# Optimization experiments

Measured on AMD Instinct MI355X. Metric: run time of the kernel, lower is better.

The kernel has to match this reference:

```python
import jax, jax.numpy as jnp
import numpy as np

NUM_HEADS = 12
DIM_HEAD = 64
SCALE = DIM_HEAD ** -0.5
LOG2PI = float(np.log(2.0 * np.pi))


def setup_inputs() -> dict:
    key = jax.random.key(0)
    k1, k2, k3, k4 = jax.random.split(key, 4)
    b, n, e = 2, 2048, 768
    inner = NUM_HEADS * DIM_HEAD
    return {
        "x": jax.random.normal(k1, (b, n, e), dtype=jnp.float32),
        "w_qkv": jax.random.normal(k2, (e, 3 * inner), dtype=jnp.float32) * (e ** -0.5),
        "w_out": jax.random.normal(k3, (inner, e), dtype=jnp.float32) * (inner ** -0.5),
        "b_out": jax.random.normal(k4, (e,), dtype=jnp.float32) * 0.02,
    }


def reference(x, w_qkv, w_out, b_out):
    b, n, _ = x.shape
    h, d = NUM_HEADS, DIM_HEAD
    qkv = x @ w_qkv  # (b, n, 3*h*d)
    q, k, v = jnp.split(qkv, 3, axis=-1)
    # (b, n, h*d) -> (b, h, n, d)
    to_heads = lambda t: t.reshape(b, n, h, d).transpose(0, 2, 1, 3)
    q, k, v = to_heads(q), to_heads(k), to_heads(v)

    dots = jnp.einsum("bhid,bhjd->bhij", q, k) * SCALE  # (b, h, n, n)
    attn = jax.nn.softmax(dots, axis=-1)
    product = jnp.einsum("bhij,bhjd->bhid", attn, v)  # (b, h, n, d)

    # cross-head statistics (torch.var is unbiased -> ddof=1)
    mean = jnp.mean(product, axis=1, keepdims=True)           # (b, 1, n, d)
    variance = jnp.var(product, axis=1, ddof=1, keepdims=True)  # (b, 1, n, d)

    log_probs = -0.5 * (LOG2PI + jnp.log(variance)
                        - 0.5 * (product - mean) ** 2 / variance)
    log_probs = jnp.sum(log_probs, axis=-1) \
        - jnp.sum(jnp.log(jnp.sqrt(variance)), axis=-1)  # (b, h, n)

    # second attn-weighted matmul, weighted by per-(b,h,n) log-likelihood
    out = jnp.einsum("bhij,bhjd->bhid", log_probs[..., None] * attn, v)
    out = out.transpose(0, 2, 1, 3).reshape(b, n, h * d)  # (b, n, h*d)
    return out @ w_out + b_out
```

## Files before the change

kernel.cpp:

```cpp
#include <hip/hip_runtime.h>

#define BB    2
#define NCTX  2048
#define EDIM  768
#define HH    12
#define DH    64
#define NQKV  2304
#define QSZ   (BB*HH*NCTX*DH)
#define GK    768
#define SCALE 0.125f
#define LOG2PI 1.8378770664093453f

typedef __bf16 bf16x8 __attribute__((ext_vector_type(8)));
typedef float  f32x4  __attribute__((ext_vector_type(4)));
typedef float  f32x16 __attribute__((ext_vector_type(16)));

#define GLOAD_LDS16(g, l)                                      \
  __builtin_amdgcn_global_load_lds(                            \
      (const __attribute__((address_space(1))) void*)(g),      \
      (__attribute__((address_space(3))) void*)(l), 16, 0, 0)

__global__ __launch_bounds__(256)
void cvt_x(const float* __restrict__ x, __bf16* __restrict__ xbf, int n8) {
  int i = blockIdx.x*256 + threadIdx.x;
  if (i < n8) {
    float4 a = *(const float4*)(x + (size_t)i*8);
    float4 b = *(const float4*)(x + (size_t)i*8 + 4);
    bf16x8 o;
    o[0]=(__bf16)a.x; o[1]=(__bf16)a.y; o[2]=(__bf16)a.z; o[3]=(__bf16)a.w;
    o[4]=(__bf16)b.x; o[5]=(__bf16)b.y; o[6]=(__bf16)b.z; o[7]=(__bf16)b.w;
    *(bf16x8*)(xbf + (size_t)i*8) = o;
  }
}

__device__ __forceinline__
void cvt_T_tile(const float* __restrict__ W, __bf16* __restrict__ WT,
                int R, int C, int c0, int r0, int t) {
  __shared__ float ts[32][33];
  const int rr = t >> 5, cc = t & 31;
  #pragma unroll
  for (int i = 0; i < 4; ++i)
    ts[rr + i*8][cc] = W[(size_t)(r0 + rr + i*8)*C + c0 + cc];
  __syncthreads();
  #pragma unroll
  for (int i = 0; i < 4; ++i)
    WT[(size_t)(c0 + rr + i*8)*R + r0 + cc] = (__bf16)ts[cc][rr + i*8];
}

__global__ __launch_bounds__(256)
void cvt_T_both(const float* __restrict__ wqkv, const float* __restrict__ wout,
                __bf16* __restrict__ wqkvT, __bf16* __restrict__ woutT) {
  int b = blockIdx.x;
  if (b < 1728) {
    cvt_T_tile(wqkv, wqkvT, GK, NQKV, (b % 72)*32, (b / 72)*32, threadIdx.x);
  } else {
    b -= 1728;
    cvt_T_tile(wout, woutT, GK, EDIM, (b % 24)*32, (b / 24)*32, threadIdx.x);
  }
}

#define GEMM_CORE(Aa, Bb, acc)                                               \
  const int lane = tid & 63, w = tid >> 6;                                   \
  const int l15 = lane & 15, g = lane >> 4;                                  \
  const int wr = w >> 1, wc = w & 1;                                         \
  const int lrow16 = lane >> 2;                                              \
  const int lsl = (lane & 3) ^ ((lane >> 3) & 3);                            \
  f32x4 acc[4][4];                                                           \
  _Pragma("unroll")                                                          \
  for (int i = 0; i < 4; ++i)                                                \
    _Pragma("unroll")                                                        \
    for (int j = 0; j < 4; ++j) acc[i][j] = (f32x4){0.f,0.f,0.f,0.f};        \
  const __bf16* Asrc = (Aa) + (size_t)(w*32 + lrow16)*GK + lsl*8;            \
  const __bf16* Bsrc = (Bb) + (size_t)(w*32 + lrow16)*GK + lsl*8;            \
  char* dstA = smem + w*2048;                                                \
  char* dstB = smem + 8192 + w*2048;                                         \
  _Pragma("unroll")                                                          \
  for (int i = 0; i < 2; ++i) {                                              \
    GLOAD_LDS16(Asrc + (size_t)i*16*GK, dstA + i*1024);                      \
    GLOAD_LDS16(Bsrc + (size_t)i*16*GK, dstB + i*1024);                      \
  }                                                                          \
  for (int ki = 0; ki < GK/32; ++ki) {                                       \
    const int c = ki & 1;                                                    \
    __syncthreads();                        \
    if (ki + 1 < GK/32) {                                                    \
      _Pragma("unroll")                                                      \
      for (int i = 0; i < 2; ++i) {                                          \
        GLOAD_LDS16(Asrc + (size_t)i*16*GK + (ki+1)*32,                      \
                    dstA + (1-c)*16384 + i*1024);                            \
        GLOAD_LDS16(Bsrc + (size_t)i*16*GK + (ki+1)*32,                      \
                    dstB + (1-c)*16384 + i*1024);                            \
      }                                                                      \
    }                                                                        \
    const char* Asc = smem + c*16384;                                        \
    const char* Bsc = Asc + 8192;                                            \
    bf16x8 af[4], bf[4];                                                     \
    _Pragma("unroll")                                                        \
    for (int mf = 0; mf < 4; ++mf) {                                         \
      int m = wr*64 + mf*16 + l15;                                           \
      af[mf] = *(const bf16x8*)(Asc + m*64 + ((g*16) ^ (((m>>1)&3)<<4)));    \
    }                                                                        \
    _Pragma("unroll")                                                        \
    for (int nf = 0; nf < 4; ++nf) {                                         \
      int n = wc*64 + nf*16 + l15;                                           \
      bf[nf] = *(const bf16x8*)(Bsc + n*64 + ((g*16) ^ (((n>>1)&3)<<4)));    \
    }                                                                        \
    __builtin_amdgcn_s_setprio(1);                                           \
    _Pragma("unroll")                                                        \
    for (int mf = 0; mf < 4; ++mf)                                           \
      _Pragma("unroll")                                                      \
      for (int nf = 0; nf < 4; ++nf)                                         \
        acc[mf][nf] = __builtin_amdgcn_mfma_f32_16x16x32_bf16(               \
            af[mf], bf[nf], acc[mf][nf], 0, 0, 0);                           \
    __builtin_amdgcn_s_setprio(0);                                           \
  }

__global__ __launch_bounds__(256)
void gemm_qkv_mfma(const __bf16* __restrict__ A, const __bf16* __restrict__ BT,
                   __bf16* __restrict__ qb, __bf16* __restrict__ kb,
                   __bf16* __restrict__ vtb) {
  __shared__ __align__(16) char smem[2*16384];
  const int tid = threadIdx.x;
  const int xcd = blockIdx.x & 7, local = blockIdx.x >> 3;
  const int mb = (xcd & 3)*8 + local/9;
  const int nb = (xcd >> 2)*9 + local%9;
  const int m0 = mb*128, n0 = nb*128;
  GEMM_CORE(A + (size_t)m0*GK, BT + (size_t)n0*GK, acc)
  #pragma unroll
  for (int mf = 0; mf < 4; ++mf)
    #pragma unroll
    for (int nf = 0; nf < 4; ++nf)
      #pragma unroll
      for (int r = 0; r < 4; ++r) {
        int m = m0 + wr*64 + mf*16 + g*4 + r;
        int c = n0 + wc*64 + nf*16 + l15;
        int b_ = m >> 11, ii = m & 2047;
        int t = c / 768;
        int rem = c - t*768;
        int head = rem >> 6, dd = rem & 63;
        float val = acc[mf][nf][r];
        if (t == 0)
          qb[((size_t)(b_*HH + head)*NCTX + ii)*DH + dd] = (__bf16)(val * SCALE);
        else if (t == 1)
          kb[((size_t)(b_*HH + head)*NCTX + ii)*DH + dd] = (__bf16)val;
        else
          vtb[((size_t)(b_*HH + head)*DH + dd)*NCTX + ii] = (__bf16)val;
      }
}

__global__ __launch_bounds__(512)
void attn_mfma(const __bf16* __restrict__ Q, const __bf16* __restrict__ K,
               const __bf16* __restrict__ Vg, float* __restrict__ P) {
  __shared__ __align__(16) char smem[2*32768];
  const int bh  = blockIdx.x;
  const int q0  = blockIdx.y * 128;
  const int tid = threadIdx.x;
  const int w = tid >> 6, lane = tid & 63;
  const int wq = w & 3, wk = w >> 2;
  const int l31 = lane & 31, hi = lane >> 5;
  const __bf16* Qb = Q  + (size_t)bh * NCTX * DH;
  const __bf16* Kb = K  + (size_t)bh * NCTX * DH;
  const __bf16* Vb = Vg + (size_t)bh * DH * NCTX;

  bf16x8 qa[4];
  {
    const __bf16* qr = Qb + (size_t)(q0 + wq*32 + l31)*DH + hi*8;
    #pragma unroll
    for (int s = 0; s < 4; ++s) qa[s] = *(const bf16x8*)(qr + s*16);
  }
  bf16x8 ones;
  #pragma unroll
  for (int j = 0; j < 8; ++j) ones[j] = (__bf16)1.0f;

  f32x16 oacc[2], lacc, zero16;
  #pragma unroll
  for (int i = 0; i < 16; ++i)
    { oacc[0][i] = 0.f; oacc[1][i] = 0.f; lacc[i] = 0.f; zero16[i] = 0.f; }

  const int lrow  = lane >> 3;
  const int lslot = (lane & 7) ^ lrow;
  const bool isK = (w < 4);
  const int wg = isK ? w : (w - 4);
  const __bf16* src0 = isK ? (Kb + (size_t)(wg*16 + lrow)*DH   + lslot*8)
                           : (Vb + (size_t)(wg*16 + lrow)*NCTX + lslot*8);
  const int dstoff = (isK ? 0 : 8192) + wg*2048;

  #define STAGE(kk_, s_) do {                                                 \
    char* sb = smem + (s_)*32768 + dstoff;                                    \
    if (isK) {                                                                \
      GLOAD_LDS16(src0 + (size_t)(kk_)*DH,          sb);                      \
      GLOAD_LDS16(src0 + (size_t)(kk_)*DH + 512,    sb + 1024);               \
      GLOAD_LDS16(src0 + (size_t)(kk_)*DH + 4096,   sb + 16384);              \
      GLOAD_LDS16(src0 + (size_t)(kk_)*DH + 4608,   sb + 16384 + 1024);       \
    } else {                                                                  \
      GLOAD_LDS16(src0 + (kk_),                     sb);                      \
      GLOAD_LDS16(src0 + (kk_) + 8*NCTX,            sb + 1024);               \
      GLOAD_LDS16(src0 + (kk_) + 64,                sb + 16384);              \
      GLOAD_LDS16(src0 + (kk_) + 64 + 8*NCTX,       sb + 16384 + 1024);       \
    }                                                                         \
  } while (0)

  #define ATTN_TILE(TB) do {                                                  \
    const char* Kl = (TB);                                                    \
    const char* Vt = (TB) + 8192;                                             \
    f32x16 sacc;                                                              \
    __builtin_amdgcn_s_setprio(1);                                            \
    {                                                                         \
      const int key = wk*32 + l31;                                            \
      const char* kbase = Kl + key*128;                                       \
      const int swz = (key&7) << 4;                                           \
      bf16x8 kf = *(const bf16x8*)(kbase + ((hi*16) ^ swz));                  \
      sacc = __builtin_amdgcn_mfma_f32_32x32x16_bf16(kf, qa[0], zero16, 0, 0, 0); \
      _Pragma("unroll")                                                       \
      for (int s = 1; s < 4; ++s) {                                           \
        kf = *(const bf16x8*)(kbase + ((s*32 + hi*16) ^ swz));                \
        sacc = __builtin_amdgcn_mfma_f32_32x32x16_bf16(kf, qa[s], sacc, 0, 0, 0); \
      }                                                                       \
    }                                                                         \
    __builtin_amdgcn_s_setprio(0);                                            \
    unsigned px0, px1, px2, px3, px4, px5, px6, px7;                          \
    {                                                                         \
      float e[16];                                                            \
      _Pragma("unroll")                                                       \
      for (int r = 0; r < 16; ++r) e[r] = __expf(sacc[r]);                    \
      CVTPK(px0, e[0],  e[1]);  CVTPK(px1, e[2],  e[3]);                      \
      CVTPK(px2, e[4],  e[5]);  CVTPK(px3, e[6],  e[7]);                      \
      CVTPK(px4, e[8],  e[9]);  CVTPK(px5, e[10], e[11]);                     \
      CVTPK(px6, e[12], e[13]); CVTPK(px7, e[14], e[15]);                     \
      asm("v_permlane32_swap_b32 %0, %1" : "+v"(px0), "+v"(px2));             \
      asm("v_permlane32_swap_b32 %0, %1" : "+v"(px1), "+v"(px3));             \
      asm("v_permlane32_swap_b32 %0, %1" : "+v"(px4), "+v"(px6));             \
      asm("v_permlane32_swap_b32 %0, %1" : "+v"(px5), "+v"(px7));             \
    }                                                                         \
    union PF { unsigned u[4]; bf16x8 v; };                                    \
    PF pf0, pf1;                                                              \
    pf0.u[0]=px0; pf0.u[1]=px1; pf0.u[2]=px2; pf0.u[3]=px3;                   \
    pf1.u[0]=px4; pf1.u[1]=px5; pf1.u[2]=px6; pf1.u[3]=px7;                   \
    __builtin_amdgcn_s_setprio(1);                                            \
    _Pragma("unroll")                                                         \
    for (int s = 0; s < 2; ++s) {                                             \
      bf16x8 pf = s ? pf1.v : pf0.v;                                          \
      lacc = __builtin_amdgcn_mfma_f32_32x32x16_bf16(pf, ones, lacc, 0, 0, 0);\
      _Pragma("unroll")                                                       \
      for (int nf = 0; nf < 2; ++nf) {                                        \
        int d = nf*32 + l31;                                                  \
        bf16x8 vf = *(const bf16x8*)(Vt + d*128 +                             \
            (((wk*32 + s*16 + hi*8)*2) ^ ((d&7)<<4)));                        \
        oacc[nf] = __builtin_amdgcn_mfma_f32_32x32x16_bf16(pf, vf, oacc[nf], 0, 0, 0); \
      }                                                                       \
    }                                                                         \
    __builtin_amdgcn_s_setprio(0);                                            \
  } while (0)

  #define CVTPK(dst, a, b) \
    asm("v_cvt_pk_bf16_f32 %0, %1, %2" : "=v"(dst) : "v"(a), "v"(b))

  STAGE(0, 0);

  for (int ts = 0; ts < NCTX/128; ++ts) {
    const int s = ts & 1;
    __syncthreads();
    if (ts + 1 < NCTX/128) STAGE((ts+1)*128, 1-s);
    const char* sb = smem + s*32768;
    ATTN_TILE(sb);
    ATTN_TILE(sb + 16384);
  }
  #undef STAGE
  #undef ATTN_TILE
  #undef CVTPK

  __syncthreads();
  float* scrO = (float*)smem;
  float* scrL = (float*)(smem + 32768);
  if (wk == 1) {
    #pragma unroll
    for (int nf = 0; nf < 2; ++nf)
      #pragma unroll
      for (int r = 0; r < 16; ++r)
        scrO[((wq*2 + nf)*16 + r)*64 + lane] = oacc[nf][r];
    #pragma unroll
    for (int r = 0; r < 16; ++r)
      scrL[(wq*16 + r)*64 + lane] = lacc[r];
  }
  __syncthreads();
  if (wk == 0) {
    #pragma unroll
    for (int r = 0; r < 16; ++r) {
      float linv = 1.0f / (lacc[r] + scrL[(wq*16 + r)*64 + lane]);
      int q = q0 + wq*32 + (r&3) + 8*(r>>2) + 4*hi;
      #pragma unroll
      for (int nf = 0; nf < 2; ++nf) {
        float o = oacc[nf][r] + scrO[((wq*2 + nf)*16 + r)*64 + lane];
        P[((size_t)bh*NCTX + q)*DH + nf*32 + l31] = o * linv;
      }
    }
  }
}

__global__ __launch_bounds__(256)
void stats_scale(const float* __restrict__ P, __bf16* __restrict__ Pbf) {
  const int bi = blockIdx.x*4 + (threadIdx.x >> 6);
  const int b_ = bi >> 11, i = bi & 2047;
  const int d = threadIdx.x & 63;
  const size_t hstride = (size_t)NCTX * DH;
  const size_t base = ((size_t)(b_*HH) * NCTX + i) * DH + d;
  float x[HH];
  #pragma unroll
  for (int h = 0; h < HH; ++h) x[h] = P[base + h*hstride];
  float sum = 0.f;
  #pragma unroll
  for (int h = 0; h < HH; ++h) sum += x[h];
  float mean = sum * (1.0f/12.0f);
  float ss = 0.f;
  #pragma unroll
  for (int h = 0; h < HH; ++h) { float t = x[h]-mean; ss += t*t; }
  float var = ss * (1.0f/11.0f);
  float lv = logf(var);
  float inv = 0.25f / var;
  __bf16* orow = Pbf + (size_t)bi * GK + d;
  #pragma unroll
  for (int h = 0; h < HH; ++h) {
    float t = x[h] - mean;
    float part = -0.5f*LOG2PI - lv + t*t*inv;
    #pragma unroll
    for (int off = 32; off; off >>= 1) part += __shfl_xor(part, off);
    orow[h*DH] = (__bf16)(part * x[h]);
  }
}

__global__ __launch_bounds__(256)
void gemm_out_mfma(const __bf16* __restrict__ A, const __bf16* __restrict__ BT,
                   const float* __restrict__ bias, float* __restrict__ out) {
  __shared__ __align__(16) char smem[2*16384];
  const int tid = threadIdx.x;
  const int xcd = blockIdx.x & 7, local = blockIdx.x >> 3;
  const int mb = (xcd & 3)*8 + local/3;
  const int nb = (xcd >> 2)*3 + local%3;
  const int m0 = mb*128, n0 = nb*128;
  GEMM_CORE(A + (size_t)m0*GK, BT + (size_t)n0*GK, acc)
  #pragma unroll
  for (int mf = 0; mf < 4; ++mf)
    #pragma unroll
    for (int nf = 0; nf < 4; ++nf)
      #pragma unroll
      for (int r = 0; r < 4; ++r) {
        int m = m0 + wr*64 + mf*16 + g*4 + r;
        int c = n0 + wc*64 + nf*16 + l15;
        out[(size_t)m*EDIM + c] = acc[mf][nf][r] + bias[c];
      }
}

extern "C" void kernel_launch(void* const* d_in, const int* in_sizes, int n_in,
                              void* d_out, int out_size, void* d_ws, size_t ws_size,
                              hipStream_t stream) {
  const float* x     = (const float*)d_in[0];
  const float* w_qkv = (const float*)d_in[1];
  const float* w_out = (const float*)d_in[2];
  const float* b_out = (const float*)d_in[3];
  float* out = (float*)d_out;

  __bf16* xbf   = (__bf16*)d_ws;
  __bf16* wqkvT = xbf   + (size_t)BB*NCTX*GK;
  __bf16* woutT = wqkvT + (size_t)NQKV*GK;
  __bf16* qb    = woutT + (size_t)EDIM*GK;
  __bf16* kb    = qb  + (size_t)QSZ;
  __bf16* vtb   = kb  + (size_t)QSZ;
  __bf16* Pbf   = vtb + (size_t)QSZ;
  float*  Pf    = (float*)(Pbf + (size_t)QSZ);

  cvt_x<<<dim3((BB*NCTX*GK/8 + 255)/256), 256, 0, stream>>>(x, xbf, BB*NCTX*GK/8);
  cvt_T_both<<<dim3(2304), 256, 0, stream>>>(w_qkv, w_out, wqkvT, woutT);
  gemm_qkv_mfma<<<dim3(576), 256, 0, stream>>>(xbf, wqkvT, qb, kb, vtb);
  attn_mfma<<<dim3(BB*HH, NCTX/128), 512, 0, stream>>>(qb, kb, vtb, Pf);
  stats_scale<<<dim3(BB*NCTX/4), 256, 0, stream>>>(Pf, Pbf);
  gemm_out_mfma<<<dim3(192), 256, 0, stream>>>(Pbf, woutT, b_out, out);
}
```

Before: 119.3 us.

## Triple-buffer GEMM LDS staging with explicit vmcnt waits

Changes the shared bf16 GEMM core used by the QKV and output projections from double to triple buffering. It prefetches two k-tiles ahead and replaces __syncthreads with a partial s_waitcnt vmcnt(4) plus a raw barrier, so global-to-LDS loads for later tiles can stay in flight during the MFMA work. LDS use grows from 32KB to 48KB per block, which may lower occupancy. The attention kernel is unchanged apart from moving a macro definition.

```diff
diff --git a/kernel.cpp b/kernel.cpp
--- a/kernel.cpp
+++ b/kernel.cpp
@@ -59,6 +59,46 @@
   }
 }
 
+#define GSTAGE(t_, b_) do {                                                  \
+    _Pragma("unroll")                                                        \
+    for (int i_ = 0; i_ < 2; ++i_) {                                         \
+      GLOAD_LDS16(Asrc + (size_t)i_*16*GK + (size_t)(t_)*32,                 \
+                  dstA + (b_)*16384 + i_*1024);                              \
+      GLOAD_LDS16(Bsrc + (size_t)i_*16*GK + (size_t)(t_)*32,                 \
+                  dstB + (b_)*16384 + i_*1024);                              \
+    } } while (0)
+
+#define GITER(ki_, c_) do {                                                  \
+    if ((ki_) < GK/32 - 1)                                                   \
+      asm volatile("s_waitcnt vmcnt(4)" ::: "memory");                       \
+    else                                                                     \
+      asm volatile("s_waitcnt vmcnt(0)" ::: "memory");                       \
+    __builtin_amdgcn_s_barrier();                                            \
+    asm volatile("" ::: "memory");                                           \
+    if ((ki_) + 2 < GK/32) GSTAGE((ki_) + 2, ((c_) + 2) % 3);                \
+    const char* Asc = smem + (c_)*16384;                                     \
+    const char* Bsc = Asc + 8192;                                            \
+    bf16x8 af[4], bf[4];                                                     \
+    _Pragma("unroll")                                                        \
+    for (int mf = 0; mf < 4; ++mf) {                                         \
+      int m = wr*64 + mf*16 + l15;                                           \
+      af[mf] = *(const bf16x8*)(Asc + m*64 + ((g*16) ^ (((m>>1)&3)<<4)));    \
+    }                                                                        \
+    _Pragma("unroll")                                                        \
+    for (int nf = 0; nf < 4; ++nf) {                                         \
+      int n = wc*64 + nf*16 + l15;                                           \
+      bf[nf] = *(const bf16x8*)(Bsc + n*64 + ((g*16) ^ (((n>>1)&3)<<4)));    \
+    }                                                                        \
+    __builtin_amdgcn_s_setprio(1);                                           \
+    _Pragma("unroll")                                                        \
+    for (int mf = 0; mf < 4; ++mf)                                           \
+      _Pragma("unroll")                                                      \
+      for (int nf = 0; nf < 4; ++nf)                                         \
+        acc[mf][nf] = __builtin_amdgcn_mfma_f32_16x16x32_bf16(               \
+            af[mf], bf[nf], acc[mf][nf], 0, 0, 0);                           \
+    __builtin_amdgcn_s_setprio(0);                                           \
+  } while (0)
+
 #define GEMM_CORE(Aa, Bb, acc)                                               \
   const int lane = tid & 63, w = tid >> 6;                                   \
   const int l15 = lane & 15, g = lane >> 4;                                  \
@@ -74,51 +114,19 @@
   const __bf16* Bsrc = (Bb) + (size_t)(w*32 + lrow16)*GK + lsl*8;            \
   char* dstA = smem + w*2048;                                                \
   char* dstB = smem + 8192 + w*2048;                                         \
-  _Pragma("unroll")                                                          \
-  for (int i = 0; i < 2; ++i) {                                              \
-    GLOAD_LDS16(Asrc + (size_t)i*16*GK, dstA + i*1024);                      \
-    GLOAD_LDS16(Bsrc + (size_t)i*16*GK, dstB + i*1024);                      \
-  }                                                                          \
-  for (int ki = 0; ki < GK/32; ++ki) {                                       \
-    const int c = ki & 1;                                                    \
-    __syncthreads();                        \
-    if (ki + 1 < GK/32) {                                                    \
-      _Pragma("unroll")                                                      \
-      for (int i = 0; i < 2; ++i) {                                          \
-        GLOAD_LDS16(Asrc + (size_t)i*16*GK + (ki+1)*32,                      \
-                    dstA + (1-c)*16384 + i*1024);                            \
-        GLOAD_LDS16(Bsrc + (size_t)i*16*GK + (ki+1)*32,                      \
-                    dstB + (1-c)*16384 + i*1024);                            \
-      }                                                                      \
-    }                                                                        \
-    const char* Asc = smem + c*16384;                                        \
-    const char* Bsc = Asc + 8192;                                            \
-    bf16x8 af[4], bf[4];                                                     \
-    _Pragma("unroll")                                                        \
-    for (int mf = 0; mf < 4; ++mf) {                                         \
-      int m = wr*64 + mf*16 + l15;                                           \
-      af[mf] = *(const bf16x8*)(Asc + m*64 + ((g*16) ^ (((m>>1)&3)<<4)));    \
-    }                                                                        \
-    _Pragma("unroll")                                                        \
-    for (int nf = 0; nf < 4; ++nf) {                                         \
-      int n = wc*64 + nf*16 + l15;                                           \
-      bf[nf] = *(const bf16x8*)(Bsc + n*64 + ((g*16) ^ (((n>>1)&3)<<4)));    \
-    }                                                                        \
-    __builtin_amdgcn_s_setprio(1);                                           \
-    _Pragma("unroll")                                                        \
-    for (int mf = 0; mf < 4; ++mf)                                           \
-      _Pragma("unroll")                                                      \
-      for (int nf = 0; nf < 4; ++nf)                                         \
-        acc[mf][nf] = __builtin_amdgcn_mfma_f32_16x16x32_bf16(               \
-            af[mf], bf[nf], acc[mf][nf], 0, 0, 0);                           \
-    __builtin_amdgcn_s_setprio(0);                                           \
+  GSTAGE(0, 0);                                                              \
+  GSTAGE(1, 1);                                                              \
+  for (int kb = 0; kb < GK/96; ++kb) {                 \
+    GITER(kb*3 + 0, 0);                                                      \
+    GITER(kb*3 + 1, 1);                                                      \
+    GITER(kb*3 + 2, 2);                                                      \
   }
 
 __global__ __launch_bounds__(256)
 void gemm_qkv_mfma(const __bf16* __restrict__ A, const __bf16* __restrict__ BT,
                    __bf16* __restrict__ qb, __bf16* __restrict__ kb,
                    __bf16* __restrict__ vtb) {
-  __shared__ __align__(16) char smem[2*16384];
+  __shared__ __align__(16) char smem[3*16384];
   const int tid = threadIdx.x;
   const int xcd = blockIdx.x & 7, local = blockIdx.x >> 3;
   const int mb = (xcd & 3)*8 + local/9;
@@ -198,6 +206,9 @@
       GLOAD_LDS16(src0 + (kk_) + 64 + 8*NCTX,       sb + 16384 + 1024);       \
     }                                                                         \
   } while (0)
+
+  #define CVTPK(dst, a, b) \
+    asm("v_cvt_pk_bf16_f32 %0, %1, %2" : "=v"(dst) : "v"(a), "v"(b))
 
   #define ATTN_TILE(TB) do {                                                  \
     const char* Kl = (TB);                                                    \
@@ -251,9 +262,6 @@
     __builtin_amdgcn_s_setprio(0);                                            \
   } while (0)
 
-  #define CVTPK(dst, a, b) \
-    asm("v_cvt_pk_bf16_f32 %0, %1, %2" : "=v"(dst) : "v"(a), "v"(b))
-
   STAGE(0, 0);
 
   for (int ts = 0; ts < NCTX/128; ++ts) {
@@ -330,7 +338,7 @@
 __global__ __launch_bounds__(256)
 void gemm_out_mfma(const __bf16* __restrict__ A, const __bf16* __restrict__ BT,
                    const float* __restrict__ bias, float* __restrict__ out) {
-  __shared__ __align__(16) char smem[2*16384];
+  __shared__ __align__(16) char smem[3*16384];
   const int tid = threadIdx.x;
   const int xcd = blockIdx.x & 7, local = blockIdx.x >> 3;
   const int mb = (xcd & 3)*8 + local/3;
```

Result: faster. 108.8 us (-8.8%).
